# Optimization experiments

Measured on AMD Instinct MI355X. Metric: run time of the kernel, lower is better.

Reference implementation:

```python
import jax, jax.numpy as jnp
import numpy as np

N = 262144
EMBED = 64            # embed_size
EDGE_H = 256          # edge_hidden_size
NODE_H = 128          # node_hidden_size
LSTM_IN = 2 * EMBED   # concat(e_v, a_v)


def setup_inputs() -> dict:
    key = jax.random.key(0)
    ks = jax.random.split(key, 14)
    s = 0.05
    return {
        "Hv_t": jax.random.normal(ks[0], (N, EDGE_H), jnp.float32),
        "hvv_t": jax.random.normal(ks[1], (N, EDGE_H), jnp.float32),
        "xv_t": jax.random.normal(ks[2], (N, 2), jnp.float32),
        "hv_tm1": jax.random.normal(ks[3], (N, NODE_H), jnp.float32),
        "cv_tm1": jax.random.normal(ks[4], (N, NODE_H), jnp.float32),
        "ts_mask": jax.random.randint(ks[5], (N, 1), 0, 2, jnp.int32),
        # pos_embed: Linear(2 -> EMBED)
        "W_pos": jax.random.normal(ks[6], (EMBED, 2), jnp.float32) * s,
        "b_pos": jax.random.normal(ks[7], (EMBED,), jnp.float32) * s,
        # hid_embed: Linear(2*EDGE_H -> EMBED)
        "W_hid": jax.random.normal(ks[8], (EMBED, 2 * EDGE_H), jnp.float32) * s,
        "b_hid": jax.random.normal(ks[9], (EMBED,), jnp.float32) * s,
        # LSTM(LSTM_IN -> NODE_H), PyTorch layout: gates order i,f,g,o
        "W_ih": jax.random.normal(ks[10], (4 * NODE_H, LSTM_IN), jnp.float32) * s,
        "b_ih": jax.random.normal(ks[11], (4 * NODE_H,), jnp.float32) * s,
        "W_hh": jax.random.normal(ks[12], (4 * NODE_H, NODE_H), jnp.float32) * s,
        "b_hh": jax.random.normal(ks[13], (4 * NODE_H,), jnp.float32) * s,
    }


def reference(Hv_t, hvv_t, xv_t, hv_tm1, cv_tm1, ts_mask,
              W_pos, b_pos, W_hid, b_hid, W_ih, b_ih, W_hh, b_hh):
    # Active-node mask (N, 1). Torch gathers active rows, runs one LSTM step,
    # and scatters back; equivalently compute everywhere and select with the mask.
    mask = (ts_mask[:, 0] == 1)[:, None]

    e_v = jax.nn.relu(xv_t @ W_pos.T + b_pos)                              # (N, EMBED)
    a_v = jax.nn.relu(jnp.concatenate([hvv_t, Hv_t], axis=1) @ W_hid.T + b_hid)  # (N, EMBED)
    x = jnp.concatenate([e_v, a_v], axis=1)                                # (N, 2*EMBED)

    # Single-step LSTM cell (PyTorch gate order: i, f, g, o)
    gates = x @ W_ih.T + b_ih + hv_tm1 @ W_hh.T + b_hh                     # (N, 4*NODE_H)
    i, f, g, o = jnp.split(gates, 4, axis=1)
    i = jax.nn.sigmoid(i)
    f = jax.nn.sigmoid(f)
    g = jnp.tanh(g)
    o = jax.nn.sigmoid(o)
    c_new = f * cv_tm1 + i * g
    h_new = o * jnp.tanh(c_new)

    hv_t = jnp.where(mask, h_new, hv_tm1)
    cv_t = jnp.where(mask, c_new, cv_tm1)
    return hv_t, cv_t
```

## Files before the change

kernel.cpp:

```cpp
#include <hip/hip_runtime.h>

#define N_NODES 262144
#define BM 64
#define NTHREADS 512

typedef short s16x8 __attribute__((ext_vector_type(8)));
typedef float f32x4 __attribute__((ext_vector_type(4)));

static __device__ __forceinline__ unsigned cvtpk(float lo, float hi) {
  unsigned r;
  asm("v_cvt_pk_bf16_f32 %0, %1, %2" : "=v"(r) : "v"(lo), "v"(hi));
  return r;
}

static __device__ __forceinline__ unsigned short f2bf(float f) {
  union { float f; unsigned u; } v; v.f = f;
  unsigned u = v.u;
  u += 0x7FFFu + ((u >> 16) & 1u);
  return (unsigned short)(u >> 16);
}

static __device__ __forceinline__ unsigned long long pack4bf(f32x4 v) {
  unsigned u0 = cvtpk(v.x, v.y);
  unsigned u1 = cvtpk(v.z, v.w);
  return (unsigned long long)u0 | ((unsigned long long)u1 << 32);
}

static __device__ __forceinline__ float fsig(float x) {
  return __builtin_amdgcn_rcpf(1.0f + __expf(-x));
}
static __device__ __forceinline__ float ftanh(float x) {
  return 2.0f * __builtin_amdgcn_rcpf(1.0f + __expf(-2.0f * x)) - 1.0f;
}

__global__ void prep_kernel(const float* __restrict__ Whid, const float* __restrict__ Wih,
                            const float* __restrict__ Whh, const float* __restrict__ bih,
                            const float* __restrict__ bhh,
                            unsigned short* __restrict__ oWh2, unsigned short* __restrict__ oW2,
                            float* __restrict__ oBias) {
  int t = blockIdx.x * 256 + threadIdx.x;
  if (t < 32768) {
    int kb = t >> 11, n = (t >> 5) & 63, ki = t & 31;
    oWh2[t] = f2bf(Whid[n * 512 + kb * 32 + ki]);
  }
  if (t < 131072) {
    int kb = t >> 14, n = (t >> 5) & 511, ki = t & 31;
    int k = kb * 32 + ki;
    float v = (k < 128) ? Wih[n * 128 + k] : Whh[n * 128 + (k - 128)];
    oW2[t] = f2bf(v);
  }
  if (t < 512) oBias[t] = bih[t] + bhh[t];
}

#define SWZA(m, b) ((((m) * 1024) + (b)) ^ (((m) & 7) << 4))
#define SWZ2(m, b) ((((m) * 512) + (b)) ^ (((m) & 7) << 4))

__global__ __launch_bounds__(NTHREADS, 4) void node_rnn_kernel(
    const float* __restrict__ Hv, const float* __restrict__ hvv,
    const float* __restrict__ xv, const float* __restrict__ hvp,
    const float* __restrict__ cvp, const int* __restrict__ tsm,
    const float* __restrict__ Wpos, const float* __restrict__ bpos,
    const float* __restrict__ bhid,
    const unsigned short* __restrict__ Wh2,
    const unsigned short* __restrict__ W2,
    const float* __restrict__ biasg,
    float* __restrict__ hvo, float* __restrict__ cvo)
{
  __shared__ __align__(16) char lds[65536];

  const int tid = threadIdx.x;
  const int w   = tid >> 6;
  const int l   = tid & 63;
  const int l15 = l & 15;
  const int lk  = l >> 4;
  const int wr  = w >> 2;
  const int wc  = w & 3;
  const int node0 = blockIdx.x * BM;
  const int d   = 16 * w + l15;

#pragma unroll
  for (int it = 0; it < 16; ++it) {
    int p = tid + it * NTHREADS;
    int m = p >> 7, ch = p & 127;
    const float* src = (ch < 64) ? (hvv + (size_t)(node0 + m) * 256 + ch * 4)
                                 : (Hv  + (size_t)(node0 + m) * 256 + (ch - 64) * 4);
    f32x4 v = *(const f32x4*)src;
    *(unsigned long long*)(lds + SWZA(m, ch * 8)) = pack4bf(v);
  }

  unsigned long long actmask = __ballot(tsm[node0 + l] == 1);

  unsigned evp[4];
#pragma unroll
  for (int it = 0; it < 4; ++it) {
    int p = tid + it * NTHREADS;
    int m = p >> 5, jp = p & 31;
    float x0 = xv[(size_t)(node0 + m) * 2 + 0];
    float x1 = xv[(size_t)(node0 + m) * 2 + 1];
    float e0 = fmaxf(x0 * Wpos[(2*jp  )*2] + x1 * Wpos[(2*jp  )*2+1] + bpos[2*jp  ], 0.f);
    float e1 = fmaxf(x0 * Wpos[(2*jp+1)*2] + x1 * Wpos[(2*jp+1)*2+1] + bpos[2*jp+1], 0.f);
    evp[it] = cvtpk(e0, e1);
  }
  f32x4 hvc[4];
#pragma unroll
  for (int it = 0; it < 4; ++it) {
    int p = tid + it * NTHREADS;
    int m = p >> 5, c4 = p & 31;
    hvc[it] = *(const f32x4*)(hvp + (size_t)(node0 + m) * 128 + c4 * 4);
  }

  __syncthreads();

  f32x4 acc[2] = {f32x4{0.f,0.f,0.f,0.f}, f32x4{0.f,0.f,0.f,0.f}};
  {
    const char* whb = (const char*)Wh2 + (wc * 16 + l15) * 64 + lk * 16;
#pragma unroll
    for (int ks = 0; ks < 16; ++ks) {
      s16x8 bf = *(const s16x8*)(whb + ks * 4096);
#pragma unroll
      for (int mi = 0; mi < 2; ++mi) {
        int m = wr * 32 + mi * 16 + l15;
        s16x8 af = *(const s16x8*)(lds + SWZA(m, ks * 64 + lk * 16));
        acc[mi] = __builtin_amdgcn_mfma_f32_16x16x32_bf16(af, bf, acc[mi], 0, 0, 0);
      }
    }
  }

  __syncthreads();

#pragma unroll
  for (int it = 0; it < 4; ++it) {
    int p = tid + it * NTHREADS;
    int m = p >> 5, jp = p & 31;
    *(unsigned*)(lds + SWZ2(m, jp * 4)) = evp[it];
  }
#pragma unroll
  for (int it = 0; it < 4; ++it) {
    int p = tid + it * NTHREADS;
    int m = p >> 5, c4 = p & 31;
    *(unsigned long long*)(lds + SWZ2(m, 256 + c4 * 8)) = pack4bf(hvc[it]);
  }
  {
    float bb = bhid[wc * 16 + l15];
    int cb = (64 + wc * 16 + l15) * 2;
#pragma unroll
    for (int mi = 0; mi < 2; ++mi) {
#pragma unroll
      for (int r = 0; r < 4; ++r) {
        int m = wr * 32 + mi * 16 + lk * 4 + r;
        float av = fmaxf(acc[mi][r] + bb, 0.0f);
        *(unsigned short*)(lds + SWZ2(m, cb)) = f2bf(av);
      }
    }
  }
  __syncthreads();

  float bs[4];
#pragma unroll
  for (int j = 0; j < 4; ++j) bs[j] = biasg[128 * j + d];

  f32x4 acc2[4][4];
#pragma unroll
  for (int mi = 0; mi < 4; ++mi)
#pragma unroll
    for (int j = 0; j < 4; ++j) acc2[mi][j] = f32x4{0.f,0.f,0.f,0.f};

#pragma unroll
  for (int kk = 0; kk < 8; ++kk) {
    s16x8 a[4];
#pragma unroll
    for (int mi = 0; mi < 4; ++mi)
      a[mi] = *(const s16x8*)(lds + SWZ2(mi * 16 + l15, kk * 64 + lk * 16));
    const char* wb = (const char*)W2 + kk * 32768 + lk * 16;
#pragma unroll
    for (int j = 0; j < 4; ++j) {
      s16x8 bf = *(const s16x8*)(wb + (size_t)(16 * w + 128 * j + l15) * 64);
#pragma unroll
      for (int mi = 0; mi < 4; ++mi)
        acc2[mi][j] = __builtin_amdgcn_mfma_f32_16x16x32_bf16(a[mi], bf, acc2[mi][j], 0, 0, 0);
    }
  }

#pragma unroll
  for (int mi = 0; mi < 4; ++mi) {
#pragma unroll
    for (int r = 0; r < 4; ++r) {
      int m = mi * 16 + lk * 4 + r;
      size_t node = (size_t)node0 + m;
      int act = (int)((actmask >> m) & 1ull);
      float gi = acc2[mi][0][r] + bs[0];
      float gf = acc2[mi][1][r] + bs[1];
      float gg = acc2[mi][2][r] + bs[2];
      float go = acc2[mi][3][r] + bs[3];
      float i_ = fsig(gi), f_ = fsig(gf), o_ = fsig(go);
      float g_ = ftanh(gg);
      float co = cvp[node * 128 + d];
      float ho = hvp[node * 128 + d];
      float cn = f_ * co + i_ * g_;
      float hn = o_ * ftanh(cn);
      hvo[node * 128 + d] = act ? hn : ho;
      cvo[node * 128 + d] = act ? cn : co;
    }
  }
}

extern "C" void kernel_launch(void* const* d_in, const int* in_sizes, int n_in,
                              void* d_out, int out_size, void* d_ws, size_t ws_size,
                              hipStream_t stream) {
  const float* Hv   = (const float*)d_in[0];
  const float* hvv  = (const float*)d_in[1];
  const float* xv   = (const float*)d_in[2];
  const float* hvp  = (const float*)d_in[3];
  const float* cvp  = (const float*)d_in[4];
  const int*   tsm  = (const int*)d_in[5];
  const float* Wpos = (const float*)d_in[6];
  const float* bpos = (const float*)d_in[7];
  const float* Whid = (const float*)d_in[8];
  const float* bhid = (const float*)d_in[9];
  const float* Wih  = (const float*)d_in[10];
  const float* bih  = (const float*)d_in[11];
  const float* Whh  = (const float*)d_in[12];
  const float* bhh  = (const float*)d_in[13];

  unsigned short* wsWh2 = (unsigned short*)d_ws;
  unsigned short* wsW2  = wsWh2 + 32768;
  float* wsBias = (float*)(wsW2 + 131072);

  prep_kernel<<<512, 256, 0, stream>>>(Whid, Wih, Whh, bih, bhh,
                                       wsWh2, wsW2, wsBias);

  float* hvo = (float*)d_out;
  float* cvo = hvo + (size_t)N_NODES * 128;
  node_rnn_kernel<<<N_NODES / BM, NTHREADS, 0, stream>>>(
      Hv, hvv, xv, hvp, cvp, tsm, Wpos, bpos, bhid,
      wsWh2, wsW2, wsBias, hvo, cvo);
}
```

Before: 296.7 us.

## Split hidden-embed GEMM into two K halves and prefetch cv into LDS

The hidden-embedding GEMM now stages only hvv into a 32KB LDS buffer. Hv is loaded into registers while the first K half is computed, then written into the same buffer for the second half. The freed 32KB of LDS holds cv_tm1 for the block, fetched early with async global_load_lds so the epilogue reads it from LDS instead of a late global load. This is meant to overlap global loads with MFMA work and hide the cv latency, at the cost of an extra barrier pair and more registers for the in-flight Hv values.

```diff
diff --git a/kernel.cpp b/kernel.cpp
--- a/kernel.cpp
+++ b/kernel.cpp
@@ -31,6 +31,12 @@
 }
 static __device__ __forceinline__ float ftanh(float x) {
   return 2.0f * __builtin_amdgcn_rcpf(1.0f + __expf(-2.0f * x)) - 1.0f;
+}
+
+static __device__ __forceinline__ void gload_lds16(const void* g, void* l) {
+  __builtin_amdgcn_global_load_lds(
+      (const __attribute__((address_space(1))) unsigned*)g,
+      (__attribute__((address_space(3))) unsigned*)l, 16, 0, 0);
 }
 
 __global__ void prep_kernel(const float* __restrict__ Whid, const float* __restrict__ Wih,
@@ -52,8 +58,7 @@
   if (t < 512) oBias[t] = bih[t] + bhh[t];
 }
 
-#define SWZA(m, b) ((((m) * 1024) + (b)) ^ (((m) & 7) << 4))
-#define SWZ2(m, b) ((((m) * 512) + (b)) ^ (((m) & 7) << 4))
+#define SWZ(m, b) ((((m) * 512) + (b)) ^ (((m) & 7) << 4))
 
 __global__ __launch_bounds__(NTHREADS, 4) void node_rnn_kernel(
     const float* __restrict__ Hv, const float* __restrict__ hvv,
@@ -67,6 +72,8 @@
     float* __restrict__ hvo, float* __restrict__ cvo)
 {
   __shared__ __align__(16) char lds[65536];
+  char* bufA  = lds;
+  char* cvlds = lds + 32768;
 
   const int tid = threadIdx.x;
   const int w   = tid >> 6;
@@ -78,14 +85,22 @@
   const int node0 = blockIdx.x * BM;
   const int d   = 16 * w + l15;
 
-#pragma unroll
-  for (int it = 0; it < 16; ++it) {
-    int p = tid + it * NTHREADS;
-    int m = p >> 7, ch = p & 127;
-    const float* src = (ch < 64) ? (hvv + (size_t)(node0 + m) * 256 + ch * 4)
-                                 : (Hv  + (size_t)(node0 + m) * 256 + (ch - 64) * 4);
-    f32x4 v = *(const f32x4*)src;
-    *(unsigned long long*)(lds + SWZA(m, ch * 8)) = pack4bf(v);
+  {
+    const char* gbase = (const char*)(cvp + (size_t)node0 * 128);
+    int o = w * 4096 + l * 16;
+#pragma unroll
+    for (int i = 0; i < 4; ++i)
+      gload_lds16(gbase + o + i * 1024, cvlds + o + i * 1024);
+  }
+
+  {
+#pragma unroll
+    for (int it = 0; it < 8; ++it) {
+      int p = tid + it * NTHREADS;
+      int m = p >> 6, ch = p & 63;
+      f32x4 v = *(const f32x4*)(hvv + (size_t)(node0 + m) * 256 + ch * 4);
+      *(unsigned long long*)(bufA + SWZ(m, ch * 8)) = pack4bf(v);
+    }
   }
 
   unsigned long long actmask = __ballot(tsm[node0 + l] == 1);
@@ -111,18 +126,44 @@
 
   __syncthreads();
 
+  f32x4 gv[8];
+#pragma unroll
+  for (int it = 0; it < 8; ++it) {
+    int p = tid + it * NTHREADS;
+    int m = p >> 6, ch = p & 63;
+    gv[it] = *(const f32x4*)(Hv + (size_t)(node0 + m) * 256 + ch * 4);
+  }
+
   f32x4 acc[2] = {f32x4{0.f,0.f,0.f,0.f}, f32x4{0.f,0.f,0.f,0.f}};
-  {
-    const char* whb = (const char*)Wh2 + (wc * 16 + l15) * 64 + lk * 16;
-#pragma unroll
-    for (int ks = 0; ks < 16; ++ks) {
-      s16x8 bf = *(const s16x8*)(whb + ks * 4096);
-#pragma unroll
-      for (int mi = 0; mi < 2; ++mi) {
-        int m = wr * 32 + mi * 16 + l15;
-        s16x8 af = *(const s16x8*)(lds + SWZA(m, ks * 64 + lk * 16));
-        acc[mi] = __builtin_amdgcn_mfma_f32_16x16x32_bf16(af, bf, acc[mi], 0, 0, 0);
-      }
+  const char* whb = (const char*)Wh2 + (wc * 16 + l15) * 64 + lk * 16;
+#pragma unroll
+  for (int ks = 0; ks < 8; ++ks) {
+    s16x8 bf = *(const s16x8*)(whb + ks * 4096);
+#pragma unroll
+    for (int mi = 0; mi < 2; ++mi) {
+      s16x8 af = *(const s16x8*)(bufA + SWZ(wr * 32 + mi * 16 + l15, ks * 64 + lk * 16));
+      acc[mi] = __builtin_amdgcn_mfma_f32_16x16x32_bf16(af, bf, acc[mi], 0, 0, 0);
+    }
+  }
+
+  __syncthreads();
+
+#pragma unroll
+  for (int it = 0; it < 8; ++it) {
+    int p = tid + it * NTHREADS;
+    int m = p >> 6, ch = p & 63;
+    *(unsigned long long*)(bufA + SWZ(m, ch * 8)) = pack4bf(gv[it]);
+  }
+
+  __syncthreads();
+
+#pragma unroll
+  for (int ks = 0; ks < 8; ++ks) {
+    s16x8 bf = *(const s16x8*)(whb + (8 + ks) * 4096);
+#pragma unroll
+    for (int mi = 0; mi < 2; ++mi) {
+      s16x8 af = *(const s16x8*)(bufA + SWZ(wr * 32 + mi * 16 + l15, ks * 64 + lk * 16));
+      acc[mi] = __builtin_amdgcn_mfma_f32_16x16x32_bf16(af, bf, acc[mi], 0, 0, 0);
     }
   }
 
@@ -132,13 +173,13 @@
   for (int it = 0; it < 4; ++it) {
     int p = tid + it * NTHREADS;
     int m = p >> 5, jp = p & 31;
-    *(unsigned*)(lds + SWZ2(m, jp * 4)) = evp[it];
+    *(unsigned*)(bufA + SWZ(m, jp * 4)) = evp[it];
   }
 #pragma unroll
   for (int it = 0; it < 4; ++it) {
     int p = tid + it * NTHREADS;
     int m = p >> 5, c4 = p & 31;
-    *(unsigned long long*)(lds + SWZ2(m, 256 + c4 * 8)) = pack4bf(hvc[it]);
+    *(unsigned long long*)(bufA + SWZ(m, 256 + c4 * 8)) = pack4bf(hvc[it]);
   }
   {
     float bb = bhid[wc * 16 + l15];
@@ -149,7 +190,7 @@
       for (int r = 0; r < 4; ++r) {
         int m = wr * 32 + mi * 16 + lk * 4 + r;
         float av = fmaxf(acc[mi][r] + bb, 0.0f);
-        *(unsigned short*)(lds + SWZ2(m, cb)) = f2bf(av);
+        *(unsigned short*)(bufA + SWZ(m, cb)) = f2bf(av);
       }
     }
   }
@@ -170,7 +211,7 @@
     s16x8 a[4];
 #pragma unroll
     for (int mi = 0; mi < 4; ++mi)
-      a[mi] = *(const s16x8*)(lds + SWZ2(mi * 16 + l15, kk * 64 + lk * 16));
+      a[mi] = *(const s16x8*)(bufA + SWZ(mi * 16 + l15, kk * 64 + lk * 16));
     const char* wb = (const char*)W2 + kk * 32768 + lk * 16;
 #pragma unroll
     for (int j = 0; j < 4; ++j) {
@@ -194,7 +235,7 @@
       float go = acc2[mi][3][r] + bs[3];
       float i_ = fsig(gi), f_ = fsig(gf), o_ = fsig(go);
       float g_ = ftanh(gg);
-      float co = cvp[node * 128 + d];
+      float co = *(const float*)(cvlds + m * 512 + d * 4);
       float ho = hvp[node * 128 + d];
       float cn = f_ * co + i_ * g_;
       float hn = o_ * ftanh(cn);
```

Result: slower. 323.3 us (+9.0%).

## Stream edge features into LDS via direct global loads with double buffering

Applied to the files above, without the earlier changes.

The edge-feature input (hvv and Hv) is now copied straight from global memory into LDS as fp32 with `global_load_lds`, in four column quarters that alternate between two 32 KB buffers. Each quarter's load is issued while the previous quarter goes through the hid_embed MFMA. The fp32 to bf16 conversion now happens when A-fragments are read from LDS, not before the store. The position-embedding loads are also hoisted ahead of the bulk copy. The aim is to overlap the large global reads with compute and skip the register round trip, at the cost of more barriers and conversion work in the inner loop.

```diff
diff --git a/kernel.cpp b/kernel.cpp
--- a/kernel.cpp
+++ b/kernel.cpp
@@ -20,17 +20,17 @@
   return (unsigned short)(u >> 16);
 }
 
-static __device__ __forceinline__ unsigned long long pack4bf(f32x4 v) {
-  unsigned u0 = cvtpk(v.x, v.y);
-  unsigned u1 = cvtpk(v.z, v.w);
-  return (unsigned long long)u0 | ((unsigned long long)u1 << 32);
-}
-
 static __device__ __forceinline__ float fsig(float x) {
   return __builtin_amdgcn_rcpf(1.0f + __expf(-x));
 }
 static __device__ __forceinline__ float ftanh(float x) {
   return 2.0f * __builtin_amdgcn_rcpf(1.0f + __expf(-2.0f * x)) - 1.0f;
+}
+
+static __device__ __forceinline__ void gload_lds16(const float* g, char* l) {
+  __builtin_amdgcn_global_load_lds(
+      (const __attribute__((address_space(1))) unsigned*)g,
+      (__attribute__((address_space(3))) unsigned*)l, 16, 0, 0);
 }
 
 __global__ void prep_kernel(const float* __restrict__ Whid, const float* __restrict__ Wih,
@@ -52,7 +52,6 @@
   if (t < 512) oBias[t] = bih[t] + bhh[t];
 }
 
-#define SWZA(m, b) ((((m) * 1024) + (b)) ^ (((m) & 7) << 4))
 #define SWZ2(m, b) ((((m) * 512) + (b)) ^ (((m) & 7) << 4))
 
 __global__ __launch_bounds__(NTHREADS, 4) void node_rnn_kernel(
@@ -78,29 +77,28 @@
   const int node0 = blockIdx.x * BM;
   const int d   = 16 * w + l15;
 
-#pragma unroll
-  for (int it = 0; it < 16; ++it) {
-    int p = tid + it * NTHREADS;
-    int m = p >> 7, ch = p & 127;
-    const float* src = (ch < 64) ? (hvv + (size_t)(node0 + m) * 256 + ch * 4)
-                                 : (Hv  + (size_t)(node0 + m) * 256 + (ch - 64) * 4);
-    f32x4 v = *(const f32x4*)src;
-    *(unsigned long long*)(lds + SWZA(m, ch * 8)) = pack4bf(v);
-  }
-
-  unsigned long long actmask = __ballot(tsm[node0 + l] == 1);
-
-  unsigned evp[4];
+  int mts = tsm[node0 + l];
+  float xa[4], xb[4];
+  f32x4 wps[4];
+  float bp0[4], bp1[4];
 #pragma unroll
   for (int it = 0; it < 4; ++it) {
     int p = tid + it * NTHREADS;
     int m = p >> 5, jp = p & 31;
-    float x0 = xv[(size_t)(node0 + m) * 2 + 0];
-    float x1 = xv[(size_t)(node0 + m) * 2 + 1];
-    float e0 = fmaxf(x0 * Wpos[(2*jp  )*2] + x1 * Wpos[(2*jp  )*2+1] + bpos[2*jp  ], 0.f);
-    float e1 = fmaxf(x0 * Wpos[(2*jp+1)*2] + x1 * Wpos[(2*jp+1)*2+1] + bpos[2*jp+1], 0.f);
-    evp[it] = cvtpk(e0, e1);
-  }
+    xa[it] = xv[(size_t)(node0 + m) * 2 + 0];
+    xb[it] = xv[(size_t)(node0 + m) * 2 + 1];
+    wps[it] = *(const f32x4*)(Wpos + 4 * jp);
+    bp0[it] = bpos[2 * jp]; bp1[it] = bpos[2 * jp + 1];
+  }
+
+#pragma unroll
+  for (int i = 0; i < 4; ++i) {
+    int o = w * 4096 + i * 1024 + l * 16;
+    int r = o >> 9;
+    int c = ((o >> 4) & 31) ^ (r & 7);
+    gload_lds16(hvv + (size_t)(node0 + r) * 256 + c * 4, lds + w * 4096 + i * 1024);
+  }
+
   f32x4 hvc[4];
 #pragma unroll
   for (int it = 0; it < 4; ++it) {
@@ -109,37 +107,79 @@
     hvc[it] = *(const f32x4*)(hvp + (size_t)(node0 + m) * 128 + c4 * 4);
   }
 
+  unsigned evp[4];
+#pragma unroll
+  for (int it = 0; it < 4; ++it) {
+    float e0 = fmaxf(xa[it] * wps[it].x + xb[it] * wps[it].y + bp0[it], 0.f);
+    float e1 = fmaxf(xa[it] * wps[it].z + xb[it] * wps[it].w + bp1[it], 0.f);
+    evp[it] = cvtpk(e0, e1);
+  }
+  unsigned long long actmask = __ballot(mts == 1);
+
   __syncthreads();
 
   f32x4 acc[2] = {f32x4{0.f,0.f,0.f,0.f}, f32x4{0.f,0.f,0.f,0.f}};
-  {
-    const char* whb = (const char*)Wh2 + (wc * 16 + l15) * 64 + lk * 16;
-#pragma unroll
-    for (int ks = 0; ks < 16; ++ks) {
-      s16x8 bf = *(const s16x8*)(whb + ks * 4096);
+  const char* whb = (const char*)Wh2 + (wc * 16 + l15) * 64 + lk * 16;
+
+#pragma unroll
+  for (int q = 0; q < 4; ++q) {
+    char* stq = lds + ((q & 1) << 15);
+
+    s16x8 wq[4];
+#pragma unroll
+    for (int ks = 0; ks < 4; ++ks)
+      wq[ks] = *(const s16x8*)(whb + (q * 4 + ks) * 4096);
+
+    if (q < 3) {
+      char* dst = lds + (((q + 1) & 1) << 15);
+      const float* srcb = ((q + 1) < 2) ? hvv : Hv;
+      int colb = ((q + 1) & 1) * 128;
+#pragma unroll
+      for (int i = 0; i < 4; ++i) {
+        int o = w * 4096 + i * 1024 + l * 16;
+        int r = o >> 9;
+        int c = ((o >> 4) & 31) ^ (r & 7);
+        gload_lds16(srcb + (size_t)(node0 + r) * 256 + colb + c * 4,
+                    dst + w * 4096 + i * 1024);
+      }
+    } else {
+#pragma unroll
+      for (int it = 0; it < 4; ++it) {
+        int p = tid + it * NTHREADS;
+        int m = p >> 5, jp = p & 31;
+        *(unsigned*)(lds + SWZ2(m, jp * 4)) = evp[it];
+      }
+#pragma unroll
+      for (int it = 0; it < 4; ++it) {
+        int p = tid + it * NTHREADS;
+        int m = p >> 5, c4 = p & 31;
+        f32x4 v = hvc[it];
+        unsigned u0 = cvtpk(v.x, v.y), u1 = cvtpk(v.z, v.w);
+        unsigned long long uu = (unsigned long long)u0 | ((unsigned long long)u1 << 32);
+        *(unsigned long long*)(lds + SWZ2(m, 256 + c4 * 8)) = uu;
+      }
+    }
+
+#pragma unroll
+    for (int ks = 0; ks < 4; ++ks) {
 #pragma unroll
       for (int mi = 0; mi < 2; ++mi) {
         int m = wr * 32 + mi * 16 + l15;
-        s16x8 af = *(const s16x8*)(lds + SWZA(m, ks * 64 + lk * 16));
-        acc[mi] = __builtin_amdgcn_mfma_f32_16x16x32_bf16(af, bf, acc[mi], 0, 0, 0);
-      }
-    }
-  }
-
-  __syncthreads();
-
-#pragma unroll
-  for (int it = 0; it < 4; ++it) {
-    int p = tid + it * NTHREADS;
-    int m = p >> 5, jp = p & 31;
-    *(unsigned*)(lds + SWZ2(m, jp * 4)) = evp[it];
-  }
-#pragma unroll
-  for (int it = 0; it < 4; ++it) {
-    int p = tid + it * NTHREADS;
-    int m = p >> 5, c4 = p & 31;
-    *(unsigned long long*)(lds + SWZ2(m, 256 + c4 * 8)) = pack4bf(hvc[it]);
-  }
+        int c0 = ks * 8 + lk * 2;
+        int a0 = m * 512 + ((c0 ^ (m & 7)) * 16);
+        int a1 = m * 512 + (((c0 + 1) ^ (m & 7)) * 16);
+        f32x4 A0 = *(const f32x4*)(stq + a0);
+        f32x4 A1 = *(const f32x4*)(stq + a1);
+        union { unsigned u[4]; s16x8 v; } t;
+        t.u[0] = cvtpk(A0.x, A0.y); t.u[1] = cvtpk(A0.z, A0.w);
+        t.u[2] = cvtpk(A1.x, A1.y); t.u[3] = cvtpk(A1.z, A1.w);
+        acc[mi] = __builtin_amdgcn_mfma_f32_16x16x32_bf16(t.v, wq[ks], acc[mi], 0, 0, 0);
+      }
+    }
+
+    if (q < 3) __syncthreads();
+  }
+
   {
     float bb = bhid[wc * 16 + l15];
     int cb = (64 + wc * 16 + l15) * 2;
```

New measurement: 290.2 us. 2.2% less time.

## Split fused node RNN into async-loaded a_v GEMM kernel and gate kernel

Applied to the files above, without the earlier changes.

Splits the fused kernel in two. The first kernel computes a_v (the 512->64 projection) using global_load_lds double-buffered async copies and writes bf16 results to workspace. The second kernel reads a_v and runs the LSTM gate GEMM and elementwise update. The aim is to remove the fused kernel's large 64KB LDS footprint and its serial load-then-compute phases, but it adds an extra intermediate write and read and one more kernel launch. It falls back to a modified fused kernel when the workspace is too small, and pack4bf now uses software rounding.

```diff
diff --git a/kernel.cpp b/kernel.cpp
--- a/kernel.cpp
+++ b/kernel.cpp
@@ -1,8 +1,6 @@
 #include <hip/hip_runtime.h>
 
 #define N_NODES 262144
-#define BM 64
-#define NTHREADS 512
 
 typedef short s16x8 __attribute__((ext_vector_type(8)));
 typedef float f32x4 __attribute__((ext_vector_type(4)));
@@ -21,8 +19,8 @@
 }
 
 static __device__ __forceinline__ unsigned long long pack4bf(f32x4 v) {
-  unsigned u0 = cvtpk(v.x, v.y);
-  unsigned u1 = cvtpk(v.z, v.w);
+  unsigned u0 = (unsigned)f2bf(v.x) | ((unsigned)f2bf(v.y) << 16);
+  unsigned u1 = (unsigned)f2bf(v.z) | ((unsigned)f2bf(v.w) << 16);
   return (unsigned long long)u0 | ((unsigned long long)u1 << 32);
 }
 
@@ -31,6 +29,12 @@
 }
 static __device__ __forceinline__ float ftanh(float x) {
   return 2.0f * __builtin_amdgcn_rcpf(1.0f + __expf(-2.0f * x)) - 1.0f;
+}
+
+static __device__ __forceinline__ void gload_lds16(const float* g, char* l) {
+  __builtin_amdgcn_global_load_lds(
+      (const __attribute__((address_space(1))) unsigned*)g,
+      (__attribute__((address_space(3))) unsigned*)l, 16, 0, 0);
 }
 
 __global__ void prep_kernel(const float* __restrict__ Whid, const float* __restrict__ Wih,
@@ -52,10 +56,177 @@
   if (t < 512) oBias[t] = bih[t] + bhh[t];
 }
 
+__global__ __launch_bounds__(256, 8) void node_av_kernel(
+    const float* __restrict__ Hv, const float* __restrict__ hvv,
+    const unsigned short* __restrict__ Wh2, const float* __restrict__ bhid,
+    unsigned short* __restrict__ av_out)
+{
+  __shared__ __align__(16) char lds[16384];
+  const int tid = threadIdx.x;
+  const int w   = tid >> 6;
+  const int l   = tid & 63;
+  const int l15 = l & 15;
+  const int lk  = l >> 4;
+  const int node0 = blockIdx.x * 64;
+  const char* WhB = (const char*)Wh2;
+
+
+#define ISSUE_CHUNK(c, buf)                                                       \
+  {                                                                               \
+    const float* srcb = ((c) < 8) ? hvv : Hv;                                     \
+    const int kcol = ((c) & 7) * 32;                                              \
+    _Pragma("unroll")                                                             \
+    for (int i = 0; i < 2; ++i) {                                                 \
+      int off = w * 2048 + i * 1024;                                              \
+      int lin = off + l * 16;                                                     \
+      int r   = lin >> 7;                                                         \
+      int c16 = (lin >> 4) & 7;                                                   \
+      int g16 = ((((c16 >> 1) ^ (r & 3)) << 1) | (c16 & 1));                      \
+      gload_lds16(srcb + (size_t)(node0 + r) * 256 + kcol + g16 * 4, (buf) + off);\
+    }                                                                             \
+  }
+
+  f32x4 acc[4] = {f32x4{0.f,0.f,0.f,0.f}, f32x4{0.f,0.f,0.f,0.f},
+                  f32x4{0.f,0.f,0.f,0.f}, f32x4{0.f,0.f,0.f,0.f}};
+
+  ISSUE_CHUNK(0, lds);
+  __syncthreads();
+
+#pragma unroll
+  for (int c = 0; c < 16; ++c) {
+    char* cur = lds + ((c & 1) << 13);
+    if (c < 15) ISSUE_CHUNK(c + 1, lds + (((c + 1) & 1) << 13));
+
+    int r = (w << 4) + l15;
+    const char* ap = cur + r * 128 + ((lk ^ (r & 3)) << 5);
+    f32x4 A0 = *(const f32x4*)ap;
+    f32x4 A1 = *(const f32x4*)(ap + 16);
+    union { unsigned u[4]; s16x8 v; } t;
+    t.u[0] = cvtpk(A0.x, A0.y); t.u[1] = cvtpk(A0.z, A0.w);
+    t.u[2] = cvtpk(A1.x, A1.y); t.u[3] = cvtpk(A1.z, A1.w);
+#pragma unroll
+    for (int nt = 0; nt < 4; ++nt) {
+      s16x8 bf = *(const s16x8*)(WhB + c * 4096 + (nt * 16 + l15) * 64 + lk * 16);
+      acc[nt] = __builtin_amdgcn_mfma_f32_16x16x32_bf16(t.v, bf, acc[nt], 0, 0, 0);
+    }
+    __syncthreads();
+  }
+
+#pragma unroll
+  for (int nt = 0; nt < 4; ++nt) {
+    int col = nt * 16 + l15;
+    float bb = bhid[col];
+#pragma unroll
+    for (int rg = 0; rg < 4; ++rg) {
+      int row = (w << 4) + (lk << 2) + rg;
+      av_out[(size_t)(node0 + row) * 64 + col] = f2bf(fmaxf(acc[nt][rg] + bb, 0.f));
+    }
+  }
+#undef ISSUE_CHUNK
+}
+
+#define SWZ2(m, b) ((((m) * 512) + (b)) ^ (((m) & 7) << 4))
+
+__global__ __launch_bounds__(512, 4) void node_gate_kernel(
+    const float* __restrict__ xv, const float* __restrict__ hvp,
+    const float* __restrict__ cvp, const int* __restrict__ tsm,
+    const float* __restrict__ Wpos, const float* __restrict__ bpos,
+    const unsigned short* __restrict__ av,
+    const unsigned short* __restrict__ W2,
+    const float* __restrict__ biasg,
+    float* __restrict__ hvo, float* __restrict__ cvo)
+{
+  __shared__ __align__(16) char lds[32768];
+
+  const int tid = threadIdx.x;
+  const int w   = tid >> 6;
+  const int l   = tid & 63;
+  const int l15 = l & 15;
+  const int lk  = l >> 4;
+  const int node0 = blockIdx.x * 64;
+  const int d   = 16 * w + l15;
+
+  {
+    int m = tid >> 3, c8 = tid & 7;
+    s16x8 va = *(const s16x8*)(av + (size_t)(node0 + m) * 64 + c8 * 8);
+    *(s16x8*)(lds + SWZ2(m, 128 + c8 * 16)) = va;
+  }
+
+  unsigned long long actmask = __ballot(tsm[node0 + l] == 1);
+
+#pragma unroll
+  for (int it = 0; it < 4; ++it) {
+    int p = tid + it * 512;
+    int m = p >> 5, jp = p & 31;
+    float x0 = xv[(size_t)(node0 + m) * 2 + 0];
+    float x1 = xv[(size_t)(node0 + m) * 2 + 1];
+    float e0 = fmaxf(x0 * Wpos[(2*jp  )*2] + x1 * Wpos[(2*jp  )*2+1] + bpos[2*jp  ], 0.f);
+    float e1 = fmaxf(x0 * Wpos[(2*jp+1)*2] + x1 * Wpos[(2*jp+1)*2+1] + bpos[2*jp+1], 0.f);
+    unsigned u = cvtpk(e0, e1);
+    *(unsigned*)(lds + SWZ2(m, jp * 4)) = u;
+  }
+#pragma unroll
+  for (int it = 0; it < 4; ++it) {
+    int p = tid + it * 512;
+    int m = p >> 5, c4 = p & 31;
+    f32x4 v = *(const f32x4*)(hvp + (size_t)(node0 + m) * 128 + c4 * 4);
+    *(unsigned long long*)(lds + SWZ2(m, 256 + c4 * 8)) = pack4bf(v);
+  }
+
+  __syncthreads();
+
+  float bs[4];
+#pragma unroll
+  for (int j = 0; j < 4; ++j) bs[j] = biasg[128 * j + d];
+
+  f32x4 acc2[4][4];
+#pragma unroll
+  for (int mi = 0; mi < 4; ++mi)
+#pragma unroll
+    for (int j = 0; j < 4; ++j) acc2[mi][j] = f32x4{0.f,0.f,0.f,0.f};
+
+#pragma unroll
+  for (int kk = 0; kk < 8; ++kk) {
+    s16x8 a[4];
+#pragma unroll
+    for (int mi = 0; mi < 4; ++mi)
+      a[mi] = *(const s16x8*)(lds + SWZ2(mi * 16 + l15, kk * 64 + lk * 16));
+    const char* wb = (const char*)W2 + kk * 32768 + lk * 16;
+#pragma unroll
+    for (int j = 0; j < 4; ++j) {
+      s16x8 bf = *(const s16x8*)(wb + (size_t)(16 * w + 128 * j + l15) * 64);
+#pragma unroll
+      for (int mi = 0; mi < 4; ++mi)
+        acc2[mi][j] = __builtin_amdgcn_mfma_f32_16x16x32_bf16(a[mi], bf, acc2[mi][j], 0, 0, 0);
+    }
+  }
+
+#pragma unroll
+  for (int mi = 0; mi < 4; ++mi) {
+#pragma unroll
+    for (int r = 0; r < 4; ++r) {
+      int m = mi * 16 + lk * 4 + r;
+      size_t node = (size_t)node0 + m;
+      int act = (int)((actmask >> m) & 1ull);
+      float gi = acc2[mi][0][r] + bs[0];
+      float gf = acc2[mi][1][r] + bs[1];
+      float gg = acc2[mi][2][r] + bs[2];
+      float go = acc2[mi][3][r] + bs[3];
+      float i_ = fsig(gi), f_ = fsig(gf), o_ = fsig(go);
+      float g_ = ftanh(gg);
+      float co = cvp[node * 128 + d];
+      float ho = hvp[node * 128 + d];
+      float cn = f_ * co + i_ * g_;
+      float hn = o_ * ftanh(cn);
+      hvo[node * 128 + d] = act ? hn : ho;
+      cvo[node * 128 + d] = act ? cn : co;
+    }
+  }
+}
+
 #define SWZA(m, b) ((((m) * 1024) + (b)) ^ (((m) & 7) << 4))
-#define SWZ2(m, b) ((((m) * 512) + (b)) ^ (((m) & 7) << 4))
-
-__global__ __launch_bounds__(NTHREADS, 4) void node_rnn_kernel(
+
+__global__ __launch_bounds__(512, 4) void node_rnn_fused(
     const float* __restrict__ Hv, const float* __restrict__ hvv,
     const float* __restrict__ xv, const float* __restrict__ hvp,
     const float* __restrict__ cvp, const int* __restrict__ tsm,
@@ -67,7 +238,6 @@
     float* __restrict__ hvo, float* __restrict__ cvo)
 {
   __shared__ __align__(16) char lds[65536];
-
   const int tid = threadIdx.x;
   const int w   = tid >> 6;
   const int l   = tid & 63;
@@ -75,40 +245,33 @@
   const int lk  = l >> 4;
   const int wr  = w >> 2;
   const int wc  = w & 3;
-  const int node0 = blockIdx.x * BM;
-  const int d   = 16 * w + l15;
+  const int node0 = blockIdx.x * 64;
 
 #pragma unroll
   for (int it = 0; it < 16; ++it) {
-    int p = tid + it * NTHREADS;
+    int p = tid + it * 512;
     int m = p >> 7, ch = p & 127;
     const float* src = (ch < 64) ? (hvv + (size_t)(node0 + m) * 256 + ch * 4)
                                  : (Hv  + (size_t)(node0 + m) * 256 + (ch - 64) * 4);
     f32x4 v = *(const f32x4*)src;
     *(unsigned long long*)(lds + SWZA(m, ch * 8)) = pack4bf(v);
   }
-
-  unsigned long long actmask = __ballot(tsm[node0 + l] == 1);
-
-  unsigned evp[4];
-#pragma unroll
-  for (int it = 0; it < 4; ++it) {
-    int p = tid + it * NTHREADS;
-    int m = p >> 5, jp = p & 31;
+  float ev[8];
+#pragma unroll
+  for (int it = 0; it < 8; ++it) {
+    int p = tid + it * 512;
+    int m = p >> 6, j = p & 63;
     float x0 = xv[(size_t)(node0 + m) * 2 + 0];
     float x1 = xv[(size_t)(node0 + m) * 2 + 1];
-    float e0 = fmaxf(x0 * Wpos[(2*jp  )*2] + x1 * Wpos[(2*jp  )*2+1] + bpos[2*jp  ], 0.f);
-    float e1 = fmaxf(x0 * Wpos[(2*jp+1)*2] + x1 * Wpos[(2*jp+1)*2+1] + bpos[2*jp+1], 0.f);
-    evp[it] = cvtpk(e0, e1);
+    ev[it] = fmaxf(x0 * Wpos[j * 2 + 0] + x1 * Wpos[j * 2 + 1] + bpos[j], 0.0f);
   }
   f32x4 hvc[4];
 #pragma unroll
   for (int it = 0; it < 4; ++it) {
-    int p = tid + it * NTHREADS;
+    int p = tid + it * 512;
     int m = p >> 5, c4 = p & 31;
     hvc[it] = *(const f32x4*)(hvp + (size_t)(node0 + m) * 128 + c4 * 4);
   }
-
   __syncthreads();
 
   f32x4 acc[2] = {f32x4{0.f,0.f,0.f,0.f}, f32x4{0.f,0.f,0.f,0.f}};
@@ -125,18 +288,17 @@
       }
     }
   }
-
   __syncthreads();
 
 #pragma unroll
+  for (int it = 0; it < 8; ++it) {
+    int p = tid + it * 512;
+    int m = p >> 6, j = p & 63;
+    *(unsigned short*)(lds + SWZ2(m, j * 2)) = f2bf(ev[it]);
+  }
+#pragma unroll
   for (int it = 0; it < 4; ++it) {
-    int p = tid + it * NTHREADS;
-    int m = p >> 5, jp = p & 31;
-    *(unsigned*)(lds + SWZ2(m, jp * 4)) = evp[it];
-  }
-#pragma unroll
-  for (int it = 0; it < 4; ++it) {
-    int p = tid + it * NTHREADS;
+    int p = tid + it * 512;
     int m = p >> 5, c4 = p & 31;
     *(unsigned long long*)(lds + SWZ2(m, 256 + c4 * 8)) = pack4bf(hvc[it]);
   }
@@ -155,16 +317,11 @@
   }
   __syncthreads();
 
-  float bs[4];
-#pragma unroll
-  for (int j = 0; j < 4; ++j) bs[j] = biasg[128 * j + d];
-
   f32x4 acc2[4][4];
 #pragma unroll
   for (int mi = 0; mi < 4; ++mi)
 #pragma unroll
     for (int j = 0; j < 4; ++j) acc2[mi][j] = f32x4{0.f,0.f,0.f,0.f};
-
 #pragma unroll
   for (int kk = 0; kk < 8; ++kk) {
     s16x8 a[4];
@@ -180,7 +337,11 @@
         acc2[mi][j] = __builtin_amdgcn_mfma_f32_16x16x32_bf16(a[mi], bf, acc2[mi][j], 0, 0, 0);
     }
   }
-
+  float bs[4];
+  const int d = 16 * w + l15;
+#pragma unroll
+  for (int j = 0; j < 4; ++j) bs[j] = biasg[128 * j + d];
+  unsigned long long actmask = __ballot(tsm[node0 + l] == 1);
 #pragma unroll
   for (int mi = 0; mi < 4; ++mi) {
 #pragma unroll
@@ -226,12 +387,23 @@
   unsigned short* wsW2  = wsWh2 + 32768;
   float* wsBias = (float*)(wsW2 + 131072);
 
+  const size_t av_off = 1 << 20;
+  const size_t need = av_off + (size_t)N_NODES * 64 * 2;
+  unsigned short* wsAv = (unsigned short*)((char*)d_ws + av_off);
+
   prep_kernel<<<512, 256, 0, stream>>>(Whid, Wih, Whh, bih, bhh,
                                        wsWh2, wsW2, wsBias);
 
   float* hvo = (float*)d_out;
   float* cvo = hvo + (size_t)N_NODES * 128;
-  node_rnn_kernel<<<N_NODES / BM, NTHREADS, 0, stream>>>(
-      Hv, hvv, xv, hvp, cvp, tsm, Wpos, bpos, bhid,
-      wsWh2, wsW2, wsBias, hvo, cvo);
-}
+
+  if (ws_size >= need) {
+    node_av_kernel<<<N_NODES / 64, 256, 0, stream>>>(Hv, hvv, wsWh2, bhid, wsAv);
+    node_gate_kernel<<<N_NODES / 64, 512, 0, stream>>>(
+        xv, hvp, cvp, tsm, Wpos, bpos, wsAv, wsW2, wsBias, hvo, cvo);
+  } else {
+    node_rnn_fused<<<N_NODES / 64, 512, 0, stream>>>(
+        Hv, hvv, xv, hvp, cvp, tsm, Wpos, bpos, bhid,
+        wsWh2, wsW2, wsBias, hvo, cvo);
+  }
+}
```

Measured after the change: 337.5 us. 13.8% more time.
